# Kernel tuning notes

Hardware: AMD Instinct MI355X
Metric: run time of the kernel (lower is better)

## Reference

```python
import jax, jax.numpy as jnp
import numpy as np

DIM = 1024
HEADS = 16
HEAD_DIM = DIM // HEADS
SCALE = HEAD_DIM ** -0.5


def setup_inputs() -> dict:
    key = jax.random.key(0)
    ks = jax.random.split(key, 9)
    b, n, m = 4, 1024, 1024
    x = jax.random.normal(ks[0], (b, n, DIM), dtype=jnp.float32)
    context = jax.random.normal(ks[1], (b, m, DIM), dtype=jnp.float32)
    mask = jax.random.randint(ks[2], (b, n, 32, 32), 0, 2, dtype=jnp.int32)
    s = DIM ** -0.5
    Wq = jax.random.normal(ks[3], (DIM, DIM), dtype=jnp.float32) * s
    bq = jnp.zeros((DIM,), dtype=jnp.float32)
    Wkv = jax.random.normal(ks[4], (DIM, 2 * DIM), dtype=jnp.float32) * s
    bkv = jnp.zeros((2 * DIM,), dtype=jnp.float32)
    Wp = jax.random.normal(ks[5], (DIM, DIM), dtype=jnp.float32) * s
    bp = jnp.zeros((DIM,), dtype=jnp.float32)
    return {"x": x, "context": context, "mask": mask,
            "Wq": Wq, "bq": bq, "Wkv": Wkv, "bkv": bkv, "Wp": Wp, "bp": bp}


def reference(x, context, mask, Wq, bq, Wkv, bkv, Wp, bp):
    b, n, _ = x.shape
    m = context.shape[1]
    h, d = HEADS, HEAD_DIM
    # projections
    q = (x @ Wq + bq).reshape(b, n, h, d).transpose(0, 2, 1, 3)       # [b,h,n,d]
    kv = (context @ Wkv + bkv).reshape(b, m, 2, h, d)
    k = kv[:, :, 0].transpose(0, 2, 1, 3)                              # [b,h,m,d]
    v = kv[:, :, 1].transpose(0, 2, 1, 3)                              # [b,h,m,d]
    dots = jnp.einsum('bhnd,bhmd->bhnm', q, k) * SCALE                 # [b,h,n,m]
    # mask: [b,n,H,W] -> [b,1,n,m]; masked_fill where mask == 0
    mflat = mask.reshape(b, n, m)[:, None]                             # [b,1,n,m]
    dots = jnp.where(mflat == 0, -jnp.inf, dots)
    attn = jax.nn.softmax(dots, axis=-1)
    out = jnp.einsum('bhnm,bhmd->bhnd', attn, v)
    out = out.transpose(0, 2, 1, 3).reshape(b, n, h * d)
    return out @ Wp + bp
```

## Files before the change

### kernel.cpp

```cpp
#include <hip/hip_runtime.h>

typedef __bf16 bf16;
typedef __bf16 bf16x8 __attribute__((ext_vector_type(8)));
typedef float f32x4 __attribute__((ext_vector_type(4)));
typedef unsigned long long u64;

#define MFMA16(a, b, c) __builtin_amdgcn_mfma_f32_16x16x32_bf16(a, b, c, 0, 0, 0)

__device__ __forceinline__ void gl_lds16(const void* g, void* l) {
  __builtin_amdgcn_global_load_lds(
      (const __attribute__((address_space(1))) unsigned int*)g,
      (__attribute__((address_space(3))) unsigned int*)l, 16, 0, 0);
}

__global__ __launch_bounds__(256)
void prep_k(const float* __restrict__ Wq, const float* __restrict__ Wkv,
            const float* __restrict__ Wp, const int* __restrict__ mask,
            const float* __restrict__ context, const float* __restrict__ x,
            bf16* __restrict__ BqkvT, bf16* __restrict__ WpT,
            u64* __restrict__ maskbits, bf16* __restrict__ cb,
            bf16* __restrict__ xb) {
  const int bx = blockIdx.x;
  const int tid = threadIdx.x;
  if (bx >= 3328) {
    const size_t i = ((size_t)(bx - 3328) * 256 + tid) * 8;
    f32x4 a0 = *(const f32x4*)(x + i);
    f32x4 a1 = *(const f32x4*)(x + i + 4);
    bf16x8 t;
#pragma unroll
    for (int j = 0; j < 4; ++j) { t[j] = (bf16)a0[j]; t[4 + j] = (bf16)a1[j]; }
    *(bf16x8*)(xb + i) = t;
    return;
  }
  if (bx >= 1280) {
    const size_t i = ((size_t)(bx - 1280) * 256 + tid) * 8;
    f32x4 a0 = *(const f32x4*)(context + i);
    f32x4 a1 = *(const f32x4*)(context + i + 4);
    bf16x8 t;
#pragma unroll
    for (int j = 0; j < 4; ++j) { t[j] = (bf16)a0[j]; t[4 + j] = (bf16)a1[j]; }
    *(bf16x8*)(cb + i) = t;
    return;
  }
  if (bx >= 1024) {
    const int idx = (bx - 1024) * 256 + tid;
    const int4* p = (const int4*)(mask + (size_t)idx * 64);
    u64 v = 0;
#pragma unroll
    for (int i = 0; i < 16; ++i) {
      int4 m = p[i];
      v |= (u64)(m.x != 0) << (4 * i);
      v |= (u64)(m.y != 0) << (4 * i + 1);
      v |= (u64)(m.z != 0) << (4 * i + 2);
      v |= (u64)(m.w != 0) << (4 * i + 3);
    }
    maskbits[idx] = v;
    return;
  }
  const int ct = bx >> 4, rt = bx & 15;
  const float* src;
  bf16* dst;
  int C, c0, drow0;
  if (ct < 16) {
    src = Wq; C = 1024; c0 = ct * 64; dst = BqkvT; drow0 = c0;
  } else if (ct < 48) {
    src = Wkv; C = 2048; c0 = (ct - 16) * 64; dst = BqkvT; drow0 = 1024 + c0;
  } else {
    src = Wp; C = 1024; c0 = (ct - 48) * 64; dst = WpT; drow0 = c0;
  }
  __shared__ bf16 T[64][72];
  const int r0 = rt * 64;
#pragma unroll
  for (int i = 0; i < 2; ++i) {
    int c = i * 256 + tid;
    int row = c >> 3, col = (c & 7) * 8;
    const float* sp = &src[(size_t)(r0 + row) * C + c0 + col];
    f32x4 a0 = *(const f32x4*)sp;
    f32x4 a1 = *(const f32x4*)(sp + 4);
    bf16x8 t;
#pragma unroll
    for (int j = 0; j < 4; ++j) { t[j] = (bf16)a0[j]; t[4 + j] = (bf16)a1[j]; }
    *(bf16x8*)&T[row][col] = t;
  }
  __syncthreads();
#pragma unroll
  for (int i = 0; i < 2; ++i) {
    int c = i * 256 + tid;
    int orow = c >> 3, ocol = (c & 7) * 8;
    bf16x8 v;
#pragma unroll
    for (int j = 0; j < 8; ++j) v[j] = T[ocol + j][orow];
    *(bf16x8*)&dst[(size_t)(drow0 + orow) * 1024 + r0 + ocol] = v;
  }
}

template <int EPI, int BN>
__global__ __launch_bounds__(256, 3)
void gemm_db2(const bf16* __restrict__ A0, const bf16* __restrict__ A1,
              const bf16* __restrict__ Bt, const float* __restrict__ bias0,
              const float* __restrict__ bias1, bf16* __restrict__ oq,
              bf16* __restrict__ ok, bf16* __restrict__ ovt,
              float* __restrict__ outf) {
  constexpr int NJ = BN / 32;
  __shared__ bf16 As[2][128][32];
  __shared__ bf16 Bs[2][BN][32];
  const int tid = threadIdx.x;
  const int lane = tid & 63;
  const int w = tid >> 6;
  const int wm = (w >> 1) * 64;
  const int wn = (w & 1) * (BN / 2);
  const int l15 = lane & 15, l4 = lane >> 4;
  const int lrow = lane >> 2;
  const int lcg = (lane & 3) ^ ((lrow >> 1) & 3);
  const int rdc = (l4 ^ ((l15 >> 1) & 3)) * 8;
  const int m0 = blockIdx.x * 128;
  const int n0 = blockIdx.y * BN;

  const bf16* Asrc = (EPI == 1) ? ((n0 < 1024) ? A0 : A1) : A0;

  f32x4 acc[4][NJ] = {};

#define STAGE(kk, buf)                                                        \
  {                                                                           \
    _Pragma("unroll") for (int it = 0; it < 2; ++it) {                        \
      const int r = w * 32 + it * 16;                                         \
      gl_lds16(&Asrc[(size_t)(m0 + r + lrow) * 1024 + (kk) + lcg * 8],        \
               &As[buf][r][0]);                                               \
    }                                                                         \
    _Pragma("unroll") for (int it = 0; it < BN / 64; ++it) {                  \
      const int r = w * (BN / 4) + it * 16;                                   \
      gl_lds16(&Bt[(size_t)(n0 + r + lrow) * 1024 + (kk) + lcg * 8],          \
               &Bs[buf][r][0]);                                               \
    }                                                                         \
  }

#define COMPUTE(buf)                                                          \
  {                                                                           \
    bf16x8 af[4], bfr[NJ];                                                    \
    _Pragma("unroll") for (int i = 0; i < 4; ++i) af[i] =                     \
        *(const bf16x8*)&As[buf][wm + i * 16 + l15][rdc];                     \
    _Pragma("unroll") for (int j = 0; j < NJ; ++j) bfr[j] =                   \
        *(const bf16x8*)&Bs[buf][wn + j * 16 + l15][rdc];                     \
    _Pragma("unroll") for (int i = 0; i < 4; ++i)                             \
        _Pragma("unroll") for (int j = 0; j < NJ; ++j) acc[i][j] =            \
            MFMA16(af[i], bfr[j], acc[i][j]);                                 \
  }

  STAGE(0, 0);
  for (int k = 0; k < 32; k += 2) {
    __syncthreads();
    STAGE((k + 1) * 32, 1);
    COMPUTE(0);
    __syncthreads();
    if (k < 30) STAGE((k + 2) * 32, 0);
    COMPUTE(1);
  }
#undef STAGE
#undef COMPUTE

  const float SCALE2 = 0.18033688011112042f;
#pragma unroll
  for (int j = 0; j < NJ; ++j) {
    const int col = n0 + wn + j * 16 + l15;
    float bc;
    if (EPI == 1) bc = (col < 1024) ? bias0[col] : bias1[col - 1024];
    else bc = bias0[col];
#pragma unroll
    for (int i = 0; i < 4; ++i) {
#pragma unroll
      for (int r = 0; r < 4; ++r) {
        const int row = m0 + wm + i * 16 + l4 * 4 + r;
        const float v = acc[i][j][r] + bc;
        if (EPI == 0) {
          outf[(size_t)row * 1024 + col] = v;
        } else {
          const int b = row >> 10, n = row & 1023;
          if (col < 1024) {
            const int h = col >> 6, d = col & 63;
            oq[(((size_t)(b * 16 + h)) * 1024 + n) * 64 + d] =
                (bf16)(v * SCALE2);
          } else {
            const int ckv = col - 1024;
            const int s = ckv >> 10, c2 = ckv & 1023;
            const int h = c2 >> 6, d = c2 & 63;
            if (s == 0)
              ok[(((size_t)(b * 16 + h)) * 1024 + n) * 64 + d] = (bf16)v;
            else
              ovt[(((size_t)(b * 16 + h)) * 64 + d) * 1024 + n] = (bf16)v;
          }
        }
      }
    }
  }
}

__global__ __launch_bounds__(256)
void attn_kernel(const bf16* __restrict__ q, const bf16* __restrict__ k,
                 const bf16* __restrict__ vT, const u64* __restrict__ maskbits,
                 bf16* __restrict__ ao) {
  const int bh = blockIdx.x;
  const int ntile = blockIdx.y;
  const int b = bh >> 4, h = bh & 15;
  const int tid = threadIdx.x;
  const int lane = tid & 63;
  const int w = tid >> 6;
  const int l15 = lane & 15, l4 = lane >> 4;

  __shared__ bf16 Ks[64][72];
  __shared__ bf16 Vts[64][72];
  __shared__ bf16 Pw[4][16][72];

  const size_t base = (size_t)bh * 65536;
  const int nrow0 = ntile * 64 + w * 16;

  bf16x8 qf[2];
#pragma unroll
  for (int ks = 0; ks < 2; ++ks)
    qf[ks] =
        *(const bf16x8*)&q[base + (size_t)(nrow0 + l15) * 64 + ks * 32 + l4 * 8];

  f32x4 o[4] = {};
  float lsum[4] = {0.0f, 0.0f, 0.0f, 0.0f};

  const u64* mb = maskbits + (size_t)(b * 1024 + nrow0) * 16;

  for (int mt = 0; mt < 16; ++mt) {
#pragma unroll
    for (int i = 0; i < 2; ++i) {
      int c = i * 256 + tid;
      int row = c >> 3, col = (c & 7) * 8;
      *(bf16x8*)&Ks[row][col] =
          *(const bf16x8*)&k[base + (size_t)(mt * 64 + row) * 64 + col];
      *(bf16x8*)&Vts[row][col] =
          *(const bf16x8*)&vT[base + (size_t)row * 1024 + mt * 64 + col];
    }
    __syncthreads();

    f32x4 s[4];
#pragma unroll
    for (int sub = 0; sub < 4; ++sub) s[sub] = f32x4{-12.f, -12.f, -12.f, -12.f};
#pragma unroll
    for (int ks = 0; ks < 2; ++ks) {
#pragma unroll
      for (int sub = 0; sub < 4; ++sub) {
        bf16x8 bfr = *(const bf16x8*)&Ks[sub * 16 + l15][ks * 32 + l4 * 8];
        s[sub] = MFMA16(qf[ks], bfr, s[sub]);
      }
    }

    u64 wbits[4];
#pragma unroll
    for (int r = 0; r < 4; ++r) wbits[r] = mb[(size_t)(l4 * 4 + r) * 16 + mt];

#pragma unroll
    for (int sub = 0; sub < 4; ++sub) {
#pragma unroll
      for (int r = 0; r < 4; ++r) {
        float p = exp2f(s[sub][r]);
        p = ((wbits[r] >> (sub * 16 + l15)) & 1) ? p : 0.0f;
        lsum[r] += p;
        Pw[w][l4 * 4 + r][sub * 16 + l15] = (bf16)p;
      }
    }

#pragma unroll
    for (int ks = 0; ks < 2; ++ks) {
      bf16x8 af = *(const bf16x8*)&Pw[w][l15][ks * 32 + l4 * 8];
#pragma unroll
      for (int sub = 0; sub < 4; ++sub) {
        bf16x8 bfr = *(const bf16x8*)&Vts[sub * 16 + l15][ks * 32 + l4 * 8];
        o[sub] = MFMA16(af, bfr, o[sub]);
      }
    }
    __syncthreads();
  }

  float inv[4];
#pragma unroll
  for (int r = 0; r < 4; ++r) {
    float t = lsum[r];
#pragma unroll
    for (int d = 1; d < 16; d <<= 1) t += __shfl_xor(t, d);
    inv[r] = 1.0f / t;
  }

#pragma unroll
  for (int sub = 0; sub < 4; ++sub) {
#pragma unroll
    for (int r = 0; r < 4; ++r) {
      const int n = nrow0 + l4 * 4 + r;
      const size_t idx =
          ((size_t)(b * 1024 + n)) * 1024 + h * 64 + sub * 16 + l15;
      ao[idx] = (bf16)(o[sub][r] * inv[r]);
    }
  }
}

extern "C" void kernel_launch(void* const* d_in, const int* in_sizes, int n_in,
                              void* d_out, int out_size, void* d_ws,
                              size_t ws_size, hipStream_t stream) {
  const float* x = (const float*)d_in[0];
  const float* context = (const float*)d_in[1];
  const int* mask = (const int*)d_in[2];
  const float* Wq = (const float*)d_in[3];
  const float* bq = (const float*)d_in[4];
  const float* Wkv = (const float*)d_in[5];
  const float* bkv = (const float*)d_in[6];
  const float* Wp = (const float*)d_in[7];
  const float* bp = (const float*)d_in[8];
  float* out = (float*)d_out;

  char* ws = (char*)d_ws;
  bf16* cb = (bf16*)(ws);
  bf16* aow = (bf16*)(ws);
  bf16* xb = (bf16*)(ws + (8ull << 20));
  bf16* BqkvT = (bf16*)(ws + (16ull << 20));
  bf16* qw = (bf16*)(ws + (22ull << 20));
  bf16* kw = (bf16*)(ws + (30ull << 20));
  bf16* vtw = (bf16*)(ws + (38ull << 20));
  u64* maskbits = (u64*)(ws + (46ull << 20));
  bf16* WpT = (bf16*)(ws + (46ull << 20) + (512ull << 10));

  const dim3 blk(256);

  prep_k<<<dim3(5376), blk, 0, stream>>>(Wq, Wkv, Wp, mask, context, x, BqkvT,
                                         WpT, maskbits, cb, xb);

  gemm_db2<1, 128><<<dim3(32, 24), blk, 0, stream>>>(xb, cb, BqkvT, bq, bkv,
                                                     qw, kw, vtw, nullptr);

  attn_kernel<<<dim3(64, 16), blk, 0, stream>>>(qw, kw, vtw, maskbits, aow);

  gemm_db2<0, 64><<<dim3(32, 16), blk, 0, stream>>>(aow, nullptr, WpT, bp,
                                                    nullptr, nullptr, nullptr,
                                                    nullptr, out);
}
```

Baseline: 219.7 us.

## Double-buffer K/V tiles via direct-to-LDS loads with swizzled layout in attention

Attention kernel now stages K and V^T tiles straight into LDS with global_load_lds into two buffers, prefetching the next tile while computing the current one, and drops one barrier per iteration. LDS rows are XOR-swizzled instead of padded to avoid bank conflicts. The QK^T MFMA operands are swapped so each lane holds a column, which makes the mask load one word per lane and the row-sum a two-step shuffle. It also adds s_setprio around MFMA blocks and occupancy hint 4; risks include swizzle index errors and the LDS write/read ordering of P.

```diff
diff --git a/kernel.cpp b/kernel.cpp
--- a/kernel.cpp
+++ b/kernel.cpp
@@ -2,6 +2,7 @@
 
 typedef __bf16 bf16;
 typedef __bf16 bf16x8 __attribute__((ext_vector_type(8)));
+typedef __bf16 bf16x4 __attribute__((ext_vector_type(4)));
 typedef float f32x4 __attribute__((ext_vector_type(4)));
 typedef unsigned long long u64;
 
@@ -194,7 +195,7 @@
   }
 }
 
-__global__ __launch_bounds__(256)
+__global__ __launch_bounds__(256, 4)
 void attn_kernel(const bf16* __restrict__ q, const bf16* __restrict__ k,
                  const bf16* __restrict__ vT, const u64* __restrict__ maskbits,
                  bf16* __restrict__ ao) {
@@ -206,9 +207,9 @@
   const int w = tid >> 6;
   const int l15 = lane & 15, l4 = lane >> 4;
 
-  __shared__ bf16 Ks[64][72];
-  __shared__ bf16 Vts[64][72];
-  __shared__ bf16 Pw[4][16][72];
+  __shared__ bf16 Ks[2][64][64];
+  __shared__ bf16 Vts[2][64][64];
+  __shared__ bf16 Pw[4][16][64];
 
   const size_t base = (size_t)bh * 65536;
   const int nrow0 = ntile * 64 + w * 16;
@@ -216,73 +217,91 @@
   bf16x8 qf[2];
 #pragma unroll
   for (int ks = 0; ks < 2; ++ks)
-    qf[ks] =
-        *(const bf16x8*)&q[base + (size_t)(nrow0 + l15) * 64 + ks * 32 + l4 * 8];
+    qf[ks] = *(const bf16x8*)&q[base + (size_t)(nrow0 + l15) * 64 + ks * 32 +
+                                l4 * 8];
+
+  const u64* mb = maskbits + (size_t)(b * 1024 + nrow0 + l15) * 16;
+
+  const int srow = lane >> 3;
+  const int sgl = (lane & 7) ^ srow;
+  const bf16* kp = &k[base + (size_t)(w * 16 + srow) * 64 + sgl * 8];
+  const bf16* vp = &vT[base + (size_t)(w * 16 + srow) * 1024 + sgl * 8];
+
+  const int rc0 = ((0 + l4) ^ (l15 & 7)) * 8;
+  const int rc1 = ((4 + l4) ^ (l15 & 7)) * 8;
 
   f32x4 o[4] = {};
-  float lsum[4] = {0.0f, 0.0f, 0.0f, 0.0f};
-
-  const u64* mb = maskbits + (size_t)(b * 1024 + nrow0) * 16;
-
+  float lsum = 0.0f;
+
+#define STAGEA(mt_, buf_)                                                     \
+  {                                                                           \
+    _Pragma("unroll") for (int it = 0; it < 2; ++it) {                        \
+      gl_lds16(kp + (size_t)((mt_)*64 + it * 8) * 64,                         \
+               &Ks[buf_][w * 16 + it * 8][0]);                                \
+      gl_lds16(vp + (size_t)(it * 8) * 1024 + (mt_)*64,                       \
+               &Vts[buf_][w * 16 + it * 8][0]);                               \
+    }                                                                         \
+  }
+
+  STAGEA(0, 0);
   for (int mt = 0; mt < 16; ++mt) {
-#pragma unroll
-    for (int i = 0; i < 2; ++i) {
-      int c = i * 256 + tid;
-      int row = c >> 3, col = (c & 7) * 8;
-      *(bf16x8*)&Ks[row][col] =
-          *(const bf16x8*)&k[base + (size_t)(mt * 64 + row) * 64 + col];
-      *(bf16x8*)&Vts[row][col] =
-          *(const bf16x8*)&vT[base + (size_t)row * 1024 + mt * 64 + col];
-    }
+    const int cur = mt & 1;
     __syncthreads();
+    if (mt < 15) STAGEA(mt + 1, cur ^ 1);
+    const u64 wmt = mb[mt];
 
     f32x4 s[4];
 #pragma unroll
-    for (int sub = 0; sub < 4; ++sub) s[sub] = f32x4{-12.f, -12.f, -12.f, -12.f};
-#pragma unroll
-    for (int ks = 0; ks < 2; ++ks) {
-#pragma unroll
-      for (int sub = 0; sub < 4; ++sub) {
-        bf16x8 bfr = *(const bf16x8*)&Ks[sub * 16 + l15][ks * 32 + l4 * 8];
-        s[sub] = MFMA16(qf[ks], bfr, s[sub]);
+    for (int sub = 0; sub < 4; ++sub)
+      s[sub] = f32x4{-12.f, -12.f, -12.f, -12.f};
+    __builtin_amdgcn_s_setprio(1);
+#pragma unroll
+    for (int sub = 0; sub < 4; ++sub) {
+      bf16x8 kf0 = *(const bf16x8*)&Ks[cur][sub * 16 + l15][rc0];
+      bf16x8 kf1 = *(const bf16x8*)&Ks[cur][sub * 16 + l15][rc1];
+      s[sub] = MFMA16(kf0, qf[0], s[sub]);
+      s[sub] = MFMA16(kf1, qf[1], s[sub]);
+    }
+    __builtin_amdgcn_s_setprio(0);
+
+#pragma unroll
+    for (int sub = 0; sub < 4; ++sub) {
+      const int kbit = sub * 16 + l4 * 4;
+      float p[4];
+#pragma unroll
+      for (int r = 0; r < 4; ++r) {
+        float e = exp2f(s[sub][r]);
+        p[r] = ((wmt >> (kbit + r)) & 1) ? e : 0.0f;
       }
-    }
-
-    u64 wbits[4];
-#pragma unroll
-    for (int r = 0; r < 4; ++r) wbits[r] = mb[(size_t)(l4 * 4 + r) * 16 + mt];
-
+      lsum += (p[0] + p[1]) + (p[2] + p[3]);
+      bf16x4 pv;
+#pragma unroll
+      for (int r = 0; r < 4; ++r) pv[r] = (bf16)p[r];
+      const int gw = sub * 2 + (l4 >> 1);
+      char* pd = (char*)&Pw[w][l15][0] + ((gw ^ (l15 & 7)) * 16 + (l4 & 1) * 8);
+      *(bf16x4*)pd = pv;
+    }
+
+    bf16x8 af0 = *(const bf16x8*)&Pw[w][l15][rc0];
+    bf16x8 af1 = *(const bf16x8*)&Pw[w][l15][rc1];
+    __builtin_amdgcn_s_setprio(1);
 #pragma unroll
     for (int sub = 0; sub < 4; ++sub) {
-#pragma unroll
-      for (int r = 0; r < 4; ++r) {
-        float p = exp2f(s[sub][r]);
-        p = ((wbits[r] >> (sub * 16 + l15)) & 1) ? p : 0.0f;
-        lsum[r] += p;
-        Pw[w][l4 * 4 + r][sub * 16 + l15] = (bf16)p;
-      }
-    }
-
-#pragma unroll
-    for (int ks = 0; ks < 2; ++ks) {
-      bf16x8 af = *(const bf16x8*)&Pw[w][l15][ks * 32 + l4 * 8];
-#pragma unroll
-      for (int sub = 0; sub < 4; ++sub) {
-        bf16x8 bfr = *(const bf16x8*)&Vts[sub * 16 + l15][ks * 32 + l4 * 8];
-        o[sub] = MFMA16(af, bfr, o[sub]);
-      }
-    }
-    __syncthreads();
-  }
-
+      bf16x8 vf0 = *(const bf16x8*)&Vts[cur][sub * 16 + l15][rc0];
+      bf16x8 vf1 = *(const bf16x8*)&Vts[cur][sub * 16 + l15][rc1];
+      o[sub] = MFMA16(af0, vf0, o[sub]);
+      o[sub] = MFMA16(af1, vf1, o[sub]);
+    }
+    __builtin_amdgcn_s_setprio(0);
+  }
+#undef STAGEA
+
+  float t = lsum;
+  t += __shfl_xor(t, 16);
+  t += __shfl_xor(t, 32);
   float inv[4];
 #pragma unroll
-  for (int r = 0; r < 4; ++r) {
-    float t = lsum[r];
-#pragma unroll
-    for (int d = 1; d < 16; d <<= 1) t += __shfl_xor(t, d);
-    inv[r] = 1.0f / t;
-  }
+  for (int r = 0; r < 4; ++r) inv[r] = 1.0f / __shfl(t, l4 * 4 + r);
 
 #pragma unroll
   for (int sub = 0; sub < 4; ++sub) {
```

Result: faster. 211.6 us (-3.7%).
